# Kernel optimization log

Measured on AMD Instinct MI355X. Metric: run time of the kernel, lower is better.

## Reference

```python
import jax, jax.numpy as jnp
import numpy as np


def _pairwise_dist(x, y):
    # x: [B, N, D], y: [B, M, D] -> [B, N, M] Euclidean distances.
    # Use ||x||^2 + ||y||^2 - 2<x,y> (gram form) to avoid the [B,N,M,D]
    # broadcast intermediate the torch code materializes.
    x2 = jnp.sum(x * x, axis=-1)  # [B, N]
    y2 = jnp.sum(y * y, axis=-1)  # [B, M]
    xy = jnp.einsum('bnd,bmd->bnm', x, y)  # [B, N, M]
    sq = x2[:, :, None] + y2[:, None, :] - 2.0 * xy
    return jnp.sqrt(jnp.maximum(sq, 1e-12))


def setup_inputs() -> dict:
    key = jax.random.key(0)
    k1, k2 = jax.random.split(key)
    B, N, M, D = 8, 4096, 4096, 64
    pred = jax.random.normal(k1, (B, N, D), dtype=jnp.float32)
    label = jax.random.normal(k2, (B, M, D), dtype=jnp.float32)
    return {"pred": pred, "label": label}


def reference(pred, label):
    dis = _pairwise_dist(pred, label)  # [B, N, M]
    dis_xy = jnp.max(jnp.min(dis, axis=2))  # max over all (b, n) of min over m
    dis_yx = jnp.max(jnp.min(dis, axis=1))  # max over all (b, m) of min over n
    return dis_xy + dis_yx
```

## Files before the change

kernel.cpp:

```cpp
#include <hip/hip_runtime.h>
#include <hip/hip_bf16.h>

#define B_ 8
#define N_ 4096
#define M_ 4096
#define D_ 64
#define BNT (B_ * N_)
#define BMT (B_ * M_)
#define TA 64
#define TB 128
#define CHUNK_TILES 8
#define MCHUNK (M_ / (TB * CHUNK_TILES))

typedef short bf16x8 __attribute__((ext_vector_type(8)));
typedef float f32x4 __attribute__((ext_vector_type(4)));

__device__ __forceinline__ unsigned short f2bf(float f) {
  __hip_bfloat16 h = __float2bfloat16(f);
  return *reinterpret_cast<unsigned short*>(&h);
}

__device__ __forceinline__ unsigned fkey(float f) {
  unsigned b = __float_as_uint(f);
  return b ^ ((unsigned)((int)b >> 31) | 0x80000000u);
}
__device__ __forceinline__ float funkey(unsigned k) {
  unsigned b = (k & 0x80000000u) ? (k ^ 0x80000000u) : ~k;
  return __uint_as_float(b);
}

__device__ __forceinline__ void gload_lds16(const void* g, void* l) {
  __builtin_amdgcn_global_load_lds(
      (const __attribute__((address_space(1))) unsigned int*)g,
      (__attribute__((address_space(3))) unsigned int*)l, 16, 0, 0);
}

template <int ROWS, bool BF>
__device__ __forceinline__ void stage_tile(const void* gsrc, unsigned short* lds,
                                           int t, int srcpat) {
  if (BF) {
    constexpr int PER_WAVE = (ROWS * 128 / 1024) / 4;
    const char* gp = (const char*)gsrc;
    int w = t >> 6;
#pragma unroll
    for (int i = 0; i < PER_WAVE; i++) {
      int q = w * PER_WAVE + i;
      gload_lds16(gp + q * 1024 + srcpat, (char*)lds + q * 1024);
    }
  } else {
    const float4* g4 = (const float4*)gsrc;
#pragma unroll
    for (int i = 0; i < ROWS * 16 / 256; i++) {
      int off = i * 256 + t;
      float4 v = g4[off];
      int row = off >> 4;
      int cb = (off & 15) * 8;
      int ba = (row * 128 + cb) ^ ((row & 7) << 4);
      ushort4 p;
      p.x = f2bf(v.x); p.y = f2bf(v.y); p.z = f2bf(v.z); p.w = f2bf(v.w);
      *(ushort4*)((char*)lds + ba) = p;
    }
  }
}

template <bool CONV>
__global__ __launch_bounds__(256) void prep_kernel(
    const float* __restrict__ pred, const float* __restrict__ label,
    unsigned short* __restrict__ predbf, unsigned short* __restrict__ labelbf,
    float* __restrict__ x2, float* __restrict__ y2,
    unsigned* __restrict__ minN, unsigned* __restrict__ minM,
    unsigned* __restrict__ gmax) {
  int t = threadIdx.x;
  int lane = t & 15;
  long row = (long)blockIdx.x * 16 + (t >> 4);
  const float4* src;
  unsigned short* bdst;
  float* ndst;
  unsigned* mdst;
  if (row < BNT) {
    src = (const float4*)(pred + row * D_);
    bdst = predbf + row * D_;
    ndst = x2 + row;
    mdst = minN + row;
  } else {
    long r2 = row - BNT;
    src = (const float4*)(label + r2 * D_);
    bdst = labelbf + r2 * D_;
    ndst = y2 + r2;
    mdst = minM + r2;
  }
  float4 v = src[lane];
  if (CONV) {
    ushort4 p;
    p.x = f2bf(v.x); p.y = f2bf(v.y); p.z = f2bf(v.z); p.w = f2bf(v.w);
    *(ushort4*)(bdst + lane * 4) = p;
  }
  float s = v.x * v.x + v.y * v.y + v.z * v.z + v.w * v.w;
  s += __shfl_xor(s, 1);
  s += __shfl_xor(s, 2);
  s += __shfl_xor(s, 4);
  s += __shfl_xor(s, 8);
  if (lane == 0) {
    *ndst = s;
    *mdst = 0xFFFFFFFFu;
  }
  if (blockIdx.x == 0 && t < 2) gmax[t] = 0u;
}

template <bool BF>
__global__ __launch_bounds__(256) void fused_kernel(
    const void* __restrict__ Asrc, const void* __restrict__ Bsrc,
    const float* __restrict__ x2g, const float* __restrict__ y2g,
    unsigned* __restrict__ minN, unsigned* __restrict__ minM) {
  __shared__ alignas(16) unsigned short As[TA * 64];
  __shared__ alignas(16) unsigned short Bs[2][TB * 64];
  __shared__ float red[4][TA];

  const int t = threadIdx.x;
  const int b = blockIdx.z;
  const int a0 = blockIdx.x * TA;
  const int tile0 = blockIdx.y * CHUNK_TILES;
  const int w = t >> 6, l = t & 63;
  const int g = l >> 4, c = l & 15;
  const int srcpat = (l >> 3) * 128 + (((l & 7) * 16) ^ ((l >> 3) << 4));

  const size_t rowbytes = BF ? 128 : 256;
  const char* Agl = (const char*)Asrc + ((size_t)b * N_ + a0) * rowbytes;
  const char* Bgl = (const char*)Bsrc + (size_t)b * M_ * rowbytes;

  stage_tile<TA, BF>(Agl, As, t, srcpat);
  stage_tile<TB, BF>(Bgl + (size_t)tile0 * TB * rowbytes, Bs[0], t, srcpat);
  __syncthreads();

  bf16x8 af[2][4];
#pragma unroll
  for (int kk = 0; kk < 2; kk++)
#pragma unroll
    for (int mi = 0; mi < 4; mi++) {
      int r = mi * 16 + c;
      int ba = (r * 128 + kk * 64 + g * 16) ^ ((r & 7) << 4);
      af[kk][mi] = *(const bf16x8*)((const char*)As + ba);
    }

  float x2v[4][4];
#pragma unroll
  for (int mi = 0; mi < 4; mi++)
#pragma unroll
    for (int e = 0; e < 4; e++)
      x2v[mi][e] = x2g[(size_t)b * N_ + a0 + mi * 16 + g * 4 + e];

  float rmin[4][4];
#pragma unroll
  for (int mi = 0; mi < 4; mi++)
#pragma unroll
    for (int e = 0; e < 4; e++) rmin[mi][e] = INFINITY;

  for (int it = 0; it < CHUNK_TILES; it++) {
    if (it + 1 < CHUNK_TILES)
      stage_tile<TB, BF>(Bgl + (size_t)(tile0 + it + 1) * TB * rowbytes,
                         Bs[(it + 1) & 1], t, srcpat);
    const char* Bcur = (const char*)Bs[it & 1];
    const int mrow_base = (tile0 + it) * TB + w * 32;

#pragma unroll
    for (int ni = 0; ni < 2; ni++) {
      float nbv = y2g[(size_t)b * M_ + mrow_base + ni * 16 + c];
      int r = w * 32 + ni * 16 + c;
      bf16x8 b0 = *(const bf16x8*)(Bcur + ((r * 128 + g * 16) ^ ((r & 7) << 4)));
      bf16x8 b1 = *(const bf16x8*)(Bcur + ((r * 128 + 64 + g * 16) ^ ((r & 7) << 4)));
      f32x4 acc[4];
#pragma unroll
      for (int mi = 0; mi < 4; mi++)
        acc[mi] = __builtin_amdgcn_mfma_f32_16x16x32_bf16(
            af[0][mi], b0, (f32x4){0.f, 0.f, 0.f, 0.f}, 0, 0, 0);
#pragma unroll
      for (int mi = 0; mi < 4; mi++)
        acc[mi] = __builtin_amdgcn_mfma_f32_16x16x32_bf16(
            af[1][mi], b1, acc[mi], 0, 0, 0);

      float cm = INFINITY;
#pragma unroll
      for (int mi = 0; mi < 4; mi++)
#pragma unroll
        for (int e = 0; e < 4; e++) {
          float m2 = -2.f * acc[mi][e];
          rmin[mi][e] = fminf(rmin[mi][e], m2 + nbv);
          cm = fminf(cm, m2 + x2v[mi][e]);
        }
      cm = fminf(cm, __shfl_xor(cm, 16));
      cm = fminf(cm, __shfl_xor(cm, 32));
      if (g == 0)
        atomicMin(&minM[(size_t)b * M_ + mrow_base + ni * 16 + c], fkey(cm));
    }
    __syncthreads();
  }

#pragma unroll
  for (int mi = 0; mi < 4; mi++)
#pragma unroll
    for (int e = 0; e < 4; e++) {
      float r = rmin[mi][e];
      r = fminf(r, __shfl_xor(r, 1));
      r = fminf(r, __shfl_xor(r, 2));
      r = fminf(r, __shfl_xor(r, 4));
      r = fminf(r, __shfl_xor(r, 8));
      rmin[mi][e] = r;
    }
  if (c == 0) {
#pragma unroll
    for (int mi = 0; mi < 4; mi++)
#pragma unroll
      for (int e = 0; e < 4; e++)
        red[w][mi * 16 + g * 4 + e] = rmin[mi][e];
  }
  __syncthreads();
  if (t < TA) {
    float m = fminf(fminf(red[0][t], red[1][t]), fminf(red[2][t], red[3][t]));
    atomicMin(&minN[(size_t)b * N_ + a0 + t], fkey(m));
  }
}

__global__ __launch_bounds__(256) void final1_kernel(
    const unsigned* __restrict__ minN, const unsigned* __restrict__ minM,
    const float* __restrict__ x2, const float* __restrict__ y2,
    unsigned* __restrict__ gmax) {
  int dir = blockIdx.x >> 6;
  int blk = blockIdx.x & 63;
  const unsigned* src = dir ? minM : minN;
  const float* nrm = dir ? y2 : x2;
  size_t base = (size_t)blk * 512;
  float mx = -INFINITY;
  for (int i = threadIdx.x; i < 512; i += 256)
    mx = fmaxf(mx, nrm[base + i] + funkey(src[base + i]));
#pragma unroll
  for (int mask = 1; mask < 64; mask <<= 1) mx = fmaxf(mx, __shfl_xor(mx, mask));
  __shared__ float sm[4];
  if ((threadIdx.x & 63) == 0) sm[threadIdx.x >> 6] = mx;
  __syncthreads();
  if (threadIdx.x == 0) {
    mx = fmaxf(fmaxf(sm[0], sm[1]), fmaxf(sm[2], sm[3]));
    atomicMax(&gmax[dir], fkey(mx));
  }
}

__global__ void final2_kernel(const unsigned* __restrict__ gmax, float* __restrict__ out) {
  if (threadIdx.x == 0)
    out[0] = sqrtf(fmaxf(funkey(gmax[0]), 1e-12f)) +
             sqrtf(fmaxf(funkey(gmax[1]), 1e-12f));
}

extern "C" void kernel_launch(void* const* d_in, const int* in_sizes, int n_in,
                              void* d_out, int out_size, void* d_ws, size_t ws_size,
                              hipStream_t stream) {
  const float* pred = (const float*)d_in[0];
  const float* label = (const float*)d_in[1];
  char* ws = (char*)d_ws;

  const size_t bfBytes = (size_t)BNT * D_ * 2;
  const size_t needFast = 2 * bfBytes + (size_t)(BNT + BMT) * 8 + 64;

  if (ws_size >= needFast) {
    unsigned short* predbf = (unsigned short*)ws;
    unsigned short* labelbf = (unsigned short*)(ws + bfBytes);
    float* x2 = (float*)(ws + 2 * bfBytes);
    float* y2 = x2 + BNT;
    unsigned* minN = (unsigned*)(y2 + BMT);
    unsigned* minM = minN + BNT;
    unsigned* gmax = minM + BMT;

    prep_kernel<true><<<(BNT + BMT) / 16, 256, 0, stream>>>(
        pred, label, predbf, labelbf, x2, y2, minN, minM, gmax);
    fused_kernel<true><<<dim3(N_ / TA, MCHUNK, B_), 256, 0, stream>>>(
        predbf, labelbf, x2, y2, minN, minM);
    final1_kernel<<<128, 256, 0, stream>>>(minN, minM, x2, y2, gmax);
    final2_kernel<<<1, 64, 0, stream>>>(gmax, (float*)d_out);
  } else {
    float* x2 = (float*)ws;
    float* y2 = x2 + BNT;
    unsigned* minN = (unsigned*)(y2 + BMT);
    unsigned* minM = minN + BNT;
    unsigned* gmax = minM + BMT;

    prep_kernel<false><<<(BNT + BMT) / 16, 256, 0, stream>>>(
        pred, label, nullptr, nullptr, x2, y2, minN, minM, gmax);
    fused_kernel<false><<<dim3(N_ / TA, MCHUNK, B_), 256, 0, stream>>>(
        pred, label, x2, y2, minN, minM);
    final1_kernel<<<128, 256, 0, stream>>>(minN, minM, x2, y2, gmax);
    final2_kernel<<<1, 64, 0, stream>>>(gmax, (float*)d_out);
  }
}
```

Before: 66.20 us.

## Halve B tile, preload y2 norms, merge final reductions into one block

The label tile per iteration shrinks to 64 rows with twice as many iterations, so each wave handles one 16-column slice, and the y2 norms for the chunk are preloaded into registers. The epilogue uses fused multiply-adds. The two final reduction kernels and the gmax atomics are replaced by a single 1024-thread block that reads all row minima with vector loads and writes the result directly. This removes a launch and the atomics, at the risk of a serial one-CU final reduction and more barriers per column in the main kernel.

```diff
diff --git a/kernel.cpp b/kernel.cpp
--- a/kernel.cpp
+++ b/kernel.cpp
@@ -8,8 +8,8 @@
 #define BNT (B_ * N_)
 #define BMT (B_ * M_)
 #define TA 64
-#define TB 128
-#define CHUNK_TILES 8
+#define TB 64
+#define CHUNK_TILES 16
 #define MCHUNK (M_ / (TB * CHUNK_TILES))
 
 typedef short bf16x8 __attribute__((ext_vector_type(8)));
@@ -68,8 +68,7 @@
     const float* __restrict__ pred, const float* __restrict__ label,
     unsigned short* __restrict__ predbf, unsigned short* __restrict__ labelbf,
     float* __restrict__ x2, float* __restrict__ y2,
-    unsigned* __restrict__ minN, unsigned* __restrict__ minM,
-    unsigned* __restrict__ gmax) {
+    unsigned* __restrict__ minN, unsigned* __restrict__ minM) {
   int t = threadIdx.x;
   int lane = t & 15;
   long row = (long)blockIdx.x * 16 + (t >> 4);
@@ -104,7 +103,6 @@
     *ndst = s;
     *mdst = 0xFFFFFFFFu;
   }
-  if (blockIdx.x == 0 && t < 2) gmax[t] = 0u;
 }
 
 template <bool BF>
@@ -128,6 +126,13 @@
   const char* Agl = (const char*)Asrc + ((size_t)b * N_ + a0) * rowbytes;
   const char* Bgl = (const char*)Bsrc + (size_t)b * M_ * rowbytes;
 
+  float y2v[CHUNK_TILES];
+  {
+    const float* yb = y2g + (size_t)b * M_ + tile0 * TB + w * 16 + c;
+#pragma unroll
+    for (int it = 0; it < CHUNK_TILES; it++) y2v[it] = yb[it * TB];
+  }
+
   stage_tile<TA, BF>(Agl, As, t, srcpat);
   stage_tile<TB, BF>(Bgl + (size_t)tile0 * TB * rowbytes, Bs[0], t, srcpat);
   __syncthreads();
@@ -155,43 +160,40 @@
 #pragma unroll
     for (int e = 0; e < 4; e++) rmin[mi][e] = INFINITY;
 
+#pragma unroll
   for (int it = 0; it < CHUNK_TILES; it++) {
     if (it + 1 < CHUNK_TILES)
       stage_tile<TB, BF>(Bgl + (size_t)(tile0 + it + 1) * TB * rowbytes,
                          Bs[(it + 1) & 1], t, srcpat);
     const char* Bcur = (const char*)Bs[it & 1];
-    const int mrow_base = (tile0 + it) * TB + w * 32;
-
-#pragma unroll
-    for (int ni = 0; ni < 2; ni++) {
-      float nbv = y2g[(size_t)b * M_ + mrow_base + ni * 16 + c];
-      int r = w * 32 + ni * 16 + c;
-      bf16x8 b0 = *(const bf16x8*)(Bcur + ((r * 128 + g * 16) ^ ((r & 7) << 4)));
-      bf16x8 b1 = *(const bf16x8*)(Bcur + ((r * 128 + 64 + g * 16) ^ ((r & 7) << 4)));
-      f32x4 acc[4];
-#pragma unroll
-      for (int mi = 0; mi < 4; mi++)
-        acc[mi] = __builtin_amdgcn_mfma_f32_16x16x32_bf16(
-            af[0][mi], b0, (f32x4){0.f, 0.f, 0.f, 0.f}, 0, 0, 0);
-#pragma unroll
-      for (int mi = 0; mi < 4; mi++)
-        acc[mi] = __builtin_amdgcn_mfma_f32_16x16x32_bf16(
-            af[1][mi], b1, acc[mi], 0, 0, 0);
-
-      float cm = INFINITY;
-#pragma unroll
-      for (int mi = 0; mi < 4; mi++)
-#pragma unroll
-        for (int e = 0; e < 4; e++) {
-          float m2 = -2.f * acc[mi][e];
-          rmin[mi][e] = fminf(rmin[mi][e], m2 + nbv);
-          cm = fminf(cm, m2 + x2v[mi][e]);
-        }
-      cm = fminf(cm, __shfl_xor(cm, 16));
-      cm = fminf(cm, __shfl_xor(cm, 32));
-      if (g == 0)
-        atomicMin(&minM[(size_t)b * M_ + mrow_base + ni * 16 + c], fkey(cm));
-    }
+
+    int r = w * 16 + c;
+    bf16x8 b0 = *(const bf16x8*)(Bcur + ((r * 128 + g * 16) ^ ((r & 7) << 4)));
+    bf16x8 b1 = *(const bf16x8*)(Bcur + ((r * 128 + 64 + g * 16) ^ ((r & 7) << 4)));
+    f32x4 acc[4];
+#pragma unroll
+    for (int mi = 0; mi < 4; mi++)
+      acc[mi] = __builtin_amdgcn_mfma_f32_16x16x32_bf16(
+          af[0][mi], b0, (f32x4){0.f, 0.f, 0.f, 0.f}, 0, 0, 0);
+#pragma unroll
+    for (int mi = 0; mi < 4; mi++)
+      acc[mi] = __builtin_amdgcn_mfma_f32_16x16x32_bf16(
+          af[1][mi], b1, acc[mi], 0, 0, 0);
+
+    float nbv = y2v[it];
+    float cm = INFINITY;
+#pragma unroll
+    for (int mi = 0; mi < 4; mi++)
+#pragma unroll
+      for (int e = 0; e < 4; e++) {
+        rmin[mi][e] = fminf(rmin[mi][e], fmaf(-2.f, acc[mi][e], nbv));
+        cm = fminf(cm, fmaf(-2.f, acc[mi][e], x2v[mi][e]));
+      }
+    cm = fminf(cm, __shfl_xor(cm, 16));
+    cm = fminf(cm, __shfl_xor(cm, 32));
+    if (g == 0)
+      atomicMin(&minM[(size_t)b * M_ + (tile0 + it) * TB + w * 16 + c], fkey(cm));
+
     __syncthreads();
   }
 
@@ -220,33 +222,38 @@
   }
 }
 
-__global__ __launch_bounds__(256) void final1_kernel(
+__global__ __launch_bounds__(1024) void final_kernel(
     const unsigned* __restrict__ minN, const unsigned* __restrict__ minM,
     const float* __restrict__ x2, const float* __restrict__ y2,
-    unsigned* __restrict__ gmax) {
-  int dir = blockIdx.x >> 6;
-  int blk = blockIdx.x & 63;
+    float* __restrict__ out) {
+  int t = threadIdx.x;
+  int dir = t >> 9;
+  int i0 = t & 511;
   const unsigned* src = dir ? minM : minN;
   const float* nrm = dir ? y2 : x2;
-  size_t base = (size_t)blk * 512;
   float mx = -INFINITY;
-  for (int i = threadIdx.x; i < 512; i += 256)
-    mx = fmaxf(mx, nrm[base + i] + funkey(src[base + i]));
+  for (int i = i0; i < BNT / 4; i += 512) {
+    uint4 k = ((const uint4*)src)[i];
+    float4 nv = ((const float4*)nrm)[i];
+    mx = fmaxf(mx, nv.x + funkey(k.x));
+    mx = fmaxf(mx, nv.y + funkey(k.y));
+    mx = fmaxf(mx, nv.z + funkey(k.z));
+    mx = fmaxf(mx, nv.w + funkey(k.w));
+  }
 #pragma unroll
   for (int mask = 1; mask < 64; mask <<= 1) mx = fmaxf(mx, __shfl_xor(mx, mask));
-  __shared__ float sm[4];
-  if ((threadIdx.x & 63) == 0) sm[threadIdx.x >> 6] = mx;
+  __shared__ float sm[16];
+  if ((t & 63) == 0) sm[t >> 6] = mx;
   __syncthreads();
-  if (threadIdx.x == 0) {
-    mx = fmaxf(fmaxf(sm[0], sm[1]), fmaxf(sm[2], sm[3]));
-    atomicMax(&gmax[dir], fkey(mx));
-  }
-}
-
-__global__ void final2_kernel(const unsigned* __restrict__ gmax, float* __restrict__ out) {
-  if (threadIdx.x == 0)
-    out[0] = sqrtf(fmaxf(funkey(gmax[0]), 1e-12f)) +
-             sqrtf(fmaxf(funkey(gmax[1]), 1e-12f));
+  if (t == 0) {
+    float a = -INFINITY, bm = -INFINITY;
+#pragma unroll
+    for (int i = 0; i < 8; i++) {
+      a = fmaxf(a, sm[i]);
+      bm = fmaxf(bm, sm[8 + i]);
+    }
+    out[0] = sqrtf(fmaxf(a, 1e-12f)) + sqrtf(fmaxf(bm, 1e-12f));
+  }
 }
 
 extern "C" void kernel_launch(void* const* d_in, const int* in_sizes, int n_in,
@@ -266,26 +273,22 @@
     float* y2 = x2 + BNT;
     unsigned* minN = (unsigned*)(y2 + BMT);
     unsigned* minM = minN + BNT;
-    unsigned* gmax = minM + BMT;
 
     prep_kernel<true><<<(BNT + BMT) / 16, 256, 0, stream>>>(
-        pred, label, predbf, labelbf, x2, y2, minN, minM, gmax);
+        pred, label, predbf, labelbf, x2, y2, minN, minM);
     fused_kernel<true><<<dim3(N_ / TA, MCHUNK, B_), 256, 0, stream>>>(
         predbf, labelbf, x2, y2, minN, minM);
-    final1_kernel<<<128, 256, 0, stream>>>(minN, minM, x2, y2, gmax);
-    final2_kernel<<<1, 64, 0, stream>>>(gmax, (float*)d_out);
+    final_kernel<<<1, 1024, 0, stream>>>(minN, minM, x2, y2, (float*)d_out);
   } else {
     float* x2 = (float*)ws;
     float* y2 = x2 + BNT;
     unsigned* minN = (unsigned*)(y2 + BMT);
     unsigned* minM = minN + BNT;
-    unsigned* gmax = minM + BMT;
 
     prep_kernel<false><<<(BNT + BMT) / 16, 256, 0, stream>>>(
-        pred, label, nullptr, nullptr, x2, y2, minN, minM, gmax);
+        pred, label, nullptr, nullptr, x2, y2, minN, minM);
     fused_kernel<false><<<dim3(N_ / TA, MCHUNK, B_), 256, 0, stream>>>(
         pred, label, x2, y2, minN, minM);
-    final1_kernel<<<128, 256, 0, stream>>>(minN, minM, x2, y2, gmax);
-    final2_kernel<<<1, 64, 0, stream>>>(gmax, (float*)d_out);
-  }
-}
+    final_kernel<<<1, 1024, 0, stream>>>(minN, minM, x2, y2, (float*)d_out);
+  }
+}
```

Result: no change. 67.35 us (+1.7%).

## Use 128x128 wave tiles, fold -2 and y2 into MFMA, batch column-min atomics

Applied to the files above, without the earlier changes.

Doubles the A tile to 128 rows with a 2x2 wave layout so each wave computes 64x64 per B tile. A fragments are loaded straight from global into registers, with no LDS staging. The -2 scale is folded into the bf16 A conversion and y2 is used as the MFMA accumulator init, which removes the per-element multiply-add. Per-column minima are collected in an LDS slab and written with one atomic per column per block instead of per tile, and final1 is vectorized. This raises register pressure (launch bounds 3) and LDS use in exchange for fewer atomics and less per-element VALU work.

```diff
diff --git a/kernel.cpp b/kernel.cpp
--- a/kernel.cpp
+++ b/kernel.cpp
@@ -7,10 +7,11 @@
 #define D_ 64
 #define BNT (B_ * N_)
 #define BMT (B_ * M_)
-#define TA 64
+#define TA 128
 #define TB 128
 #define CHUNK_TILES 8
-#define MCHUNK (M_ / (TB * CHUNK_TILES))
+#define CHUNK_B (TB * CHUNK_TILES)
+#define MCHUNK (M_ / CHUNK_B)
 
 typedef short bf16x8 __attribute__((ext_vector_type(8)));
 typedef float f32x4 __attribute__((ext_vector_type(4)));
@@ -27,6 +28,13 @@
 __device__ __forceinline__ float funkey(unsigned k) {
   unsigned b = (k & 0x80000000u) ? (k ^ 0x80000000u) : ~k;
   return __uint_as_float(b);
+}
+
+__device__ __forceinline__ bf16x8 cvt8(float4 lo, float4 hi) {
+  union { unsigned short u[8]; bf16x8 v; } r;
+  r.u[0] = f2bf(lo.x); r.u[1] = f2bf(lo.y); r.u[2] = f2bf(lo.z); r.u[3] = f2bf(lo.w);
+  r.u[4] = f2bf(hi.x); r.u[5] = f2bf(hi.y); r.u[6] = f2bf(hi.z); r.u[7] = f2bf(hi.w);
+  return r.v;
 }
 
 __device__ __forceinline__ void gload_lds16(const void* g, void* l) {
@@ -73,11 +81,12 @@
   int t = threadIdx.x;
   int lane = t & 15;
   long row = (long)blockIdx.x * 16 + (t >> 4);
+  bool isA = row < BNT;
   const float4* src;
   unsigned short* bdst;
   float* ndst;
   unsigned* mdst;
-  if (row < BNT) {
+  if (isA) {
     src = (const float4*)(pred + row * D_);
     bdst = predbf + row * D_;
     ndst = x2 + row;
@@ -91,8 +100,10 @@
   }
   float4 v = src[lane];
   if (CONV) {
+    float s = isA ? -2.f : 1.f;
     ushort4 p;
-    p.x = f2bf(v.x); p.y = f2bf(v.y); p.z = f2bf(v.z); p.w = f2bf(v.w);
+    p.x = f2bf(s * v.x); p.y = f2bf(s * v.y);
+    p.z = f2bf(s * v.z); p.w = f2bf(s * v.w);
     *(ushort4*)(bdst + lane * 4) = p;
   }
   float s = v.x * v.x + v.y * v.y + v.z * v.z + v.w * v.w;
@@ -108,89 +119,130 @@
 }
 
 template <bool BF>
-__global__ __launch_bounds__(256) void fused_kernel(
+__global__ __launch_bounds__(256, 3) void fused_kernel(
     const void* __restrict__ Asrc, const void* __restrict__ Bsrc,
     const float* __restrict__ x2g, const float* __restrict__ y2g,
     unsigned* __restrict__ minN, unsigned* __restrict__ minM) {
-  __shared__ alignas(16) unsigned short As[TA * 64];
   __shared__ alignas(16) unsigned short Bs[2][TB * 64];
-  __shared__ float red[4][TA];
+  __shared__ float y2l[CHUNK_B];
+  __shared__ float cmSlab[2][CHUNK_B];
+  __shared__ float red[2][TA];
 
   const int t = threadIdx.x;
   const int b = blockIdx.z;
   const int a0 = blockIdx.x * TA;
-  const int tile0 = blockIdx.y * CHUNK_TILES;
+  const int m0 = blockIdx.y * CHUNK_B;
   const int w = t >> 6, l = t & 63;
   const int g = l >> 4, c = l & 15;
+  const int wr = w >> 1, wc = w & 1;
   const int srcpat = (l >> 3) * 128 + (((l & 7) * 16) ^ ((l >> 3) << 4));
 
   const size_t rowbytes = BF ? 128 : 256;
-  const char* Agl = (const char*)Asrc + ((size_t)b * N_ + a0) * rowbytes;
-  const char* Bgl = (const char*)Bsrc + (size_t)b * M_ * rowbytes;
-
-  stage_tile<TA, BF>(Agl, As, t, srcpat);
-  stage_tile<TB, BF>(Bgl + (size_t)tile0 * TB * rowbytes, Bs[0], t, srcpat);
+  const char* Bgl = (const char*)Bsrc + ((size_t)b * M_ + m0) * rowbytes;
+
+  ((float4*)y2l)[t] = ((const float4*)(y2g + (size_t)b * M_ + m0))[t];
+
+  stage_tile<TB, BF>(Bgl, Bs[0], t, srcpat);
+
+  bf16x8 af[2][4];
+  if (BF) {
+    const unsigned short* Ab =
+        (const unsigned short*)Asrc + ((size_t)b * N_ + a0) * D_;
+#pragma unroll
+    for (int kk = 0; kk < 2; kk++)
+#pragma unroll
+      for (int mi = 0; mi < 4; mi++)
+        af[kk][mi] =
+            *(const bf16x8*)(Ab + (size_t)(wr * 64 + mi * 16 + c) * D_ + kk * 32 + g * 8);
+  } else {
+    const float* Af = (const float*)Asrc + ((size_t)b * N_ + a0) * D_;
+#pragma unroll
+    for (int kk = 0; kk < 2; kk++)
+#pragma unroll
+      for (int mi = 0; mi < 4; mi++) {
+        const float4* p =
+            (const float4*)(Af + (size_t)(wr * 64 + mi * 16 + c) * D_ + kk * 32 + g * 8);
+        float4 lo = p[0], hi = p[1];
+        lo.x *= -2.f; lo.y *= -2.f; lo.z *= -2.f; lo.w *= -2.f;
+        hi.x *= -2.f; hi.y *= -2.f; hi.z *= -2.f; hi.w *= -2.f;
+        af[kk][mi] = cvt8(lo, hi);
+      }
+  }
+
+  float x2v[4][4];
+#pragma unroll
+  for (int mi = 0; mi < 4; mi++)
+#pragma unroll
+    for (int e = 0; e < 4; e++)
+      x2v[mi][e] = x2g[(size_t)b * N_ + a0 + wr * 64 + mi * 16 + g * 4 + e];
+
+  float rmin[4][4];
+#pragma unroll
+  for (int mi = 0; mi < 4; mi++)
+#pragma unroll
+    for (int e = 0; e < 4; e++) rmin[mi][e] = INFINITY;
+
   __syncthreads();
 
-  bf16x8 af[2][4];
-#pragma unroll
-  for (int kk = 0; kk < 2; kk++)
-#pragma unroll
-    for (int mi = 0; mi < 4; mi++) {
-      int r = mi * 16 + c;
-      int ba = (r * 128 + kk * 64 + g * 16) ^ ((r & 7) << 4);
-      af[kk][mi] = *(const bf16x8*)((const char*)As + ba);
-    }
-
-  float x2v[4][4];
-#pragma unroll
-  for (int mi = 0; mi < 4; mi++)
-#pragma unroll
-    for (int e = 0; e < 4; e++)
-      x2v[mi][e] = x2g[(size_t)b * N_ + a0 + mi * 16 + g * 4 + e];
-
-  float rmin[4][4];
-#pragma unroll
-  for (int mi = 0; mi < 4; mi++)
-#pragma unroll
-    for (int e = 0; e < 4; e++) rmin[mi][e] = INFINITY;
-
+#pragma unroll
   for (int it = 0; it < CHUNK_TILES; it++) {
     if (it + 1 < CHUNK_TILES)
-      stage_tile<TB, BF>(Bgl + (size_t)(tile0 + it + 1) * TB * rowbytes,
+      stage_tile<TB, BF>(Bgl + (size_t)(it + 1) * TB * rowbytes,
                          Bs[(it + 1) & 1], t, srcpat);
     const char* Bcur = (const char*)Bs[it & 1];
-    const int mrow_base = (tile0 + it) * TB + w * 32;
-
-#pragma unroll
-    for (int ni = 0; ni < 2; ni++) {
-      float nbv = y2g[(size_t)b * M_ + mrow_base + ni * 16 + c];
-      int r = w * 32 + ni * 16 + c;
-      bf16x8 b0 = *(const bf16x8*)(Bcur + ((r * 128 + g * 16) ^ ((r & 7) << 4)));
-      bf16x8 b1 = *(const bf16x8*)(Bcur + ((r * 128 + 64 + g * 16) ^ ((r & 7) << 4)));
-      f32x4 acc[4];
+
+    float nbv[4];
+#pragma unroll
+    for (int ni = 0; ni < 4; ni++)
+      nbv[ni] = y2l[it * TB + wc * 64 + ni * 16 + c];
+
+#pragma unroll
+    for (int h = 0; h < 2; h++) {
+      bf16x8 b0[2], b1[2];
+#pragma unroll
+      for (int nj = 0; nj < 2; nj++) {
+        int r = wc * 64 + (h * 2 + nj) * 16 + c;
+        b0[nj] = *(const bf16x8*)(Bcur + ((r * 128 + g * 16) ^ ((r & 7) << 4)));
+        b1[nj] = *(const bf16x8*)(Bcur + ((r * 128 + 64 + g * 16) ^ ((r & 7) << 4)));
+      }
+      f32x4 acc[4][2];
 #pragma unroll
       for (int mi = 0; mi < 4; mi++)
-        acc[mi] = __builtin_amdgcn_mfma_f32_16x16x32_bf16(
-            af[0][mi], b0, (f32x4){0.f, 0.f, 0.f, 0.f}, 0, 0, 0);
+#pragma unroll
+        for (int nj = 0; nj < 2; nj++) {
+          float nv = nbv[h * 2 + nj];
+          acc[mi][nj] = (f32x4){nv, nv, nv, nv};
+        }
 #pragma unroll
       for (int mi = 0; mi < 4; mi++)
-        acc[mi] = __builtin_amdgcn_mfma_f32_16x16x32_bf16(
-            af[1][mi], b1, acc[mi], 0, 0, 0);
-
-      float cm = INFINITY;
+#pragma unroll
+        for (int nj = 0; nj < 2; nj++)
+          acc[mi][nj] = __builtin_amdgcn_mfma_f32_16x16x32_bf16(
+              af[0][mi], b0[nj], acc[mi][nj], 0, 0, 0);
 #pragma unroll
       for (int mi = 0; mi < 4; mi++)
 #pragma unroll
-        for (int e = 0; e < 4; e++) {
-          float m2 = -2.f * acc[mi][e];
-          rmin[mi][e] = fminf(rmin[mi][e], m2 + nbv);
-          cm = fminf(cm, m2 + x2v[mi][e]);
-        }
-      cm = fminf(cm, __shfl_xor(cm, 16));
-      cm = fminf(cm, __shfl_xor(cm, 32));
-      if (g == 0)
-        atomicMin(&minM[(size_t)b * M_ + mrow_base + ni * 16 + c], fkey(cm));
+        for (int nj = 0; nj < 2; nj++)
+          acc[mi][nj] = __builtin_amdgcn_mfma_f32_16x16x32_bf16(
+              af[1][mi], b1[nj], acc[mi][nj], 0, 0, 0);
+
+#pragma unroll
+      for (int nj = 0; nj < 2; nj++) {
+        float cm = INFINITY;
+#pragma unroll
+        for (int mi = 0; mi < 4; mi++)
+#pragma unroll
+          for (int e = 0; e < 4; e++) {
+            float v = acc[mi][nj][e];
+            rmin[mi][e] = fminf(rmin[mi][e], v);
+            cm = fminf(cm, v + x2v[mi][e]);
+          }
+        cm = fminf(cm, __shfl_xor(cm, 16));
+        cm = fminf(cm, __shfl_xor(cm, 32));
+        if (g == 0)
+          cmSlab[wr][it * TB + wc * 64 + (h * 2 + nj) * 16 + c] =
+              cm - nbv[h * 2 + nj];
+      }
     }
     __syncthreads();
   }
@@ -211,12 +263,18 @@
     for (int mi = 0; mi < 4; mi++)
 #pragma unroll
       for (int e = 0; e < 4; e++)
-        red[w][mi * 16 + g * 4 + e] = rmin[mi][e];
+        red[wc][wr * 64 + mi * 16 + g * 4 + e] = rmin[mi][e];
   }
   __syncthreads();
   if (t < TA) {
-    float m = fminf(fminf(red[0][t], red[1][t]), fminf(red[2][t], red[3][t]));
+    float m = fminf(red[0][t], red[1][t]);
     atomicMin(&minN[(size_t)b * N_ + a0 + t], fkey(m));
+  }
+#pragma unroll
+  for (int i = 0; i < CHUNK_B / 256; i++) {
+    int r = i * 256 + t;
+    float v = fminf(cmSlab[0][r], cmSlab[1][r]);
+    atomicMin(&minM[(size_t)b * M_ + m0 + r], fkey(v));
   }
 }
 
@@ -224,14 +282,20 @@
     const unsigned* __restrict__ minN, const unsigned* __restrict__ minM,
     const float* __restrict__ x2, const float* __restrict__ y2,
     unsigned* __restrict__ gmax) {
-  int dir = blockIdx.x >> 6;
-  int blk = blockIdx.x & 63;
+  int dir = blockIdx.x >> 5;
+  int blk = blockIdx.x & 31;
   const unsigned* src = dir ? minM : minN;
   const float* nrm = dir ? y2 : x2;
-  size_t base = (size_t)blk * 512;
+  size_t base = (size_t)blk * 256;
   float mx = -INFINITY;
-  for (int i = threadIdx.x; i < 512; i += 256)
-    mx = fmaxf(mx, nrm[base + i] + funkey(src[base + i]));
+  for (int i = threadIdx.x; i < 256; i += 256) {
+    uint4 k = ((const uint4*)src)[base + i];
+    float4 nv = ((const float4*)nrm)[base + i];
+    mx = fmaxf(mx, nv.x + funkey(k.x));
+    mx = fmaxf(mx, nv.y + funkey(k.y));
+    mx = fmaxf(mx, nv.z + funkey(k.z));
+    mx = fmaxf(mx, nv.w + funkey(k.w));
+  }
 #pragma unroll
   for (int mask = 1; mask < 64; mask <<= 1) mx = fmaxf(mx, __shfl_xor(mx, mask));
   __shared__ float sm[4];
@@ -272,7 +336,7 @@
         pred, label, predbf, labelbf, x2, y2, minN, minM, gmax);
     fused_kernel<true><<<dim3(N_ / TA, MCHUNK, B_), 256, 0, stream>>>(
         predbf, labelbf, x2, y2, minN, minM);
-    final1_kernel<<<128, 256, 0, stream>>>(minN, minM, x2, y2, gmax);
+    final1_kernel<<<64, 256, 0, stream>>>(minN, minM, x2, y2, gmax);
     final2_kernel<<<1, 64, 0, stream>>>(gmax, (float*)d_out);
   } else {
     float* x2 = (float*)ws;
@@ -285,7 +349,7 @@
         pred, label, nullptr, nullptr, x2, y2, minN, minM, gmax);
     fused_kernel<false><<<dim3(N_ / TA, MCHUNK, B_), 256, 0, stream>>>(
         pred, label, x2, y2, minN, minM);
-    final1_kernel<<<128, 256, 0, stream>>>(minN, minM, x2, y2, gmax);
+    final1_kernel<<<64, 256, 0, stream>>>(minN, minM, x2, y2, gmax);
     final2_kernel<<<1, 64, 0, stream>>>(gmax, (float*)d_out);
   }
 }
```

New measurement: 215.9 us. 3.26x slower.
